# Optimization experiments

Measured on AMD Instinct MI355X. Metric: run time of the kernel, lower is better.

The kernel has to match this reference:

```python
import jax, jax.numpy as jnp
import numpy as np

DIM = 192
TDIM = 192
HEADS = 6
WS = (2, 7, 7)
SS = (1, 3, 3)
MLP_HID = 4 * DIM
RANK = DIM // 8
EPS = 1e-6


def _rel_pos_index(ws):
    wd, wh, ww = ws
    coords = np.stack(np.meshgrid(np.arange(wd), np.arange(wh), np.arange(ww), indexing='ij'))
    cf = coords.reshape(3, -1)
    rel = (cf[:, :, None] - cf[:, None, :]).transpose(1, 2, 0).astype(np.int64)
    rel[..., 0] += wd - 1
    rel[..., 1] += wh - 1
    rel[..., 2] += ww - 1
    rel[..., 0] *= (2 * wh - 1) * (2 * ww - 1)
    rel[..., 1] *= (2 * ww - 1)
    return rel.sum(-1)  # (N, N)


def _window_partition(x, ws):
    B, D, H, W, C = x.shape
    x = x.reshape(B, D // ws[0], ws[0], H // ws[1], ws[1], W // ws[2], ws[2], C)
    return x.transpose(0, 1, 3, 5, 2, 4, 6, 7).reshape(-1, ws[0] * ws[1] * ws[2], C)


def _window_reverse(w, ws, B, D, H, W):
    x = w.reshape(B, D // ws[0], H // ws[1], W // ws[2], ws[0], ws[1], ws[2], -1)
    return x.transpose(0, 1, 4, 2, 5, 3, 6, 7).reshape(B, D, H, W, -1)


def _ln(x):
    m = x.mean(-1, keepdims=True)
    v = ((x - m) ** 2).mean(-1, keepdims=True)
    return (x - m) * jax.lax.rsqrt(v + EPS)


def _compute_mask_np(Dp, Hp, Wp, ws, ss):
    img = np.zeros((1, Dp, Hp, Wp, 1), dtype=np.float32)
    cnt = 0
    for d in (slice(0, -ws[0]), slice(-ws[0], -ss[0]), slice(-ss[0], None)):
        for h in (slice(0, -ws[1]), slice(-ws[1], -ss[1]), slice(-ss[1], None)):
            for w in (slice(0, -ws[2]), slice(-ws[2], -ss[2]), slice(-ss[2], None)):
                img[:, d, h, w, :] = cnt
                cnt += 1
    x = img.reshape(1, Dp // ws[0], ws[0], Hp // ws[1], ws[1], Wp // ws[2], ws[2], 1)
    mw = x.transpose(0, 1, 3, 5, 2, 4, 6, 7).reshape(-1, ws[0] * ws[1] * ws[2])
    am = mw[:, None, :] - mw[:, :, None]
    return np.where(am != 0, np.float32(-100.0), np.float32(0.0))


def setup_inputs() -> dict:
    key = jax.random.key(0)
    ks = jax.random.split(key, 16)
    B, D, H, W, C = 1, 16, 64, 128, DIM
    Dp = D + (-D) % WS[0]
    Hp = H + (-H) % WS[1]
    Wp = W + (-W) % WS[2]
    s = 0.02
    bias_tab = (2 * WS[0] - 1) * (2 * WS[1] - 1) * (2 * WS[2] - 1)
    return {
        'x': jax.random.normal(ks[0], (B, D, H, W, C), jnp.float32),
        'mask_matrix': jnp.asarray(_compute_mask_np(Dp, Hp, Wp, WS, SS)),
        't': jax.random.normal(ks[1], (B, TDIM), jnp.float32),
        'w_qkv': jax.random.normal(ks[2], (C, 3 * C), jnp.float32) * s,
        'b_qkv': jnp.zeros((3 * C,), jnp.float32),
        'rel_bias': jax.random.normal(ks[3], (bias_tab, HEADS), jnp.float32) * s,
        'w_proj': jax.random.normal(ks[4], (C, C), jnp.float32) * s,
        'b_proj': jnp.zeros((C,), jnp.float32),
        'w1': jax.random.normal(ks[5], (C, MLP_HID), jnp.float32) * s,
        'b1': jnp.zeros((MLP_HID,), jnp.float32),
        'w2': jax.random.normal(ks[6], (MLP_HID, C), jnp.float32) * s,
        'b2': jnp.zeros((C,), jnp.float32),
        'wa1': jax.random.normal(ks[7], (TDIM, RANK), jnp.float32) * s,
        'wa2': jax.random.normal(ks[8], (RANK, 6 * C), jnp.float32) * s,
        'ba2': jax.random.normal(ks[9], (6 * C,), jnp.float32) * s,
    }


def reference(x, mask_matrix, t, w_qkv, b_qkv, rel_bias, w_proj, b_proj, w1, b1, w2, b2, wa1, wa2, ba2):
    B, D, H, W, C = x.shape
    hd = C // HEADS
    # AdaLN modulation params
    mod = (jax.nn.silu(t) @ wa1) @ wa2 + ba2  # (B, 6C)
    sh_msa, sc_msa, g_msa, sh_mlp, sc_mlp, g_mlp = jnp.split(mod, 6, axis=1)

    def modulate(y, sh, sc):
        return y * (1 + sc[:, None, None, None, :]) + sh[:, None, None, None, :]

    shortcut = x
    y = modulate(_ln(x), sh_msa, sc_msa)
    # pad to window multiples
    pad_d, pad_h, pad_w = (-D) % WS[0], (-H) % WS[1], (-W) % WS[2]
    y = jnp.pad(y, ((0, 0), (0, pad_d), (0, pad_h), (0, pad_w), (0, 0)))
    Dp, Hp, Wp = D + pad_d, H + pad_h, W + pad_w
    # cyclic shift
    y = jnp.roll(y, (-SS[0], -SS[1], -SS[2]), axis=(1, 2, 3))
    xw = _window_partition(y, WS)  # (B*nW, N, C)
    N = xw.shape[1]
    qkv = (xw @ w_qkv + b_qkv).reshape(-1, N, 3, HEADS, hd)
    q, k, v = qkv[:, :, 0], qkv[:, :, 1], qkv[:, :, 2]
    scale = hd ** -0.5
    attn = jnp.einsum('bnhd,bmhd->bhnm', q * scale, k)  # (B*nW, H, N, N)
    rpi = _rel_pos_index(WS)
    bias = rel_bias[rpi.reshape(-1)].reshape(N, N, HEADS).transpose(2, 0, 1)
    attn = attn + bias[None]
    nW = mask_matrix.shape[0]
    attn = attn.reshape(B, nW, HEADS, N, N) + mask_matrix[None, :, None]
    attn = jax.nn.softmax(attn, axis=-1).reshape(-1, HEADS, N, N)
    out = jnp.einsum('bhnm,bmhd->bnhd', attn, v).reshape(-1, N, C)
    out = out @ w_proj + b_proj
    y = _window_reverse(out, WS, B, Dp, Hp, Wp)
    y = jnp.roll(y, (SS[0], SS[1], SS[2]), axis=(1, 2, 3))
    y = y[:, :D, :H, :W, :]
    x1 = shortcut + g_msa[:, None, None, None, :] * y
    y2 = modulate(_ln(x1), sh_mlp, sc_mlp)
    h = jax.nn.gelu(y2 @ w1 + b1, approximate=False) @ w2 + b2
    return x1 + g_mlp[:, None, None, None, :] * h
```

## Files before the change

kernel.cpp:

```cpp
#include <hip/hip_runtime.h>
#include <hip/hip_bf16.h>

typedef __bf16 bf16x8 __attribute__((ext_vector_type(8)));
typedef float  f32x4  __attribute__((ext_vector_type(4)));
typedef unsigned int u32x4 __attribute__((ext_vector_type(4)));
typedef __attribute__((address_space(3))) unsigned int lds_u32;
typedef const __attribute__((address_space(1))) unsigned int glb_u32;

__device__ inline unsigned short f2bf(float f) {
    union { __hip_bfloat16 h; unsigned short u; } cv;
    cv.h = __float2bfloat16(f);
    return cv.u;
}
__device__ inline float bf2f(unsigned short u) {
    union { unsigned int i; float f; } c; c.i = ((unsigned int)u) << 16; return c.f;
}

__device__ inline bf16x8 load8(const unsigned short* p) {
    uint2 lo = *(const uint2*)(p);
    uint2 hi = *(const uint2*)(p + 16);
    u32x4 v; v[0] = lo.x; v[1] = lo.y; v[2] = hi.x; v[3] = hi.y;
    return __builtin_bit_cast(bf16x8, v);
}

__device__ inline bf16x8 load8s(const unsigned short* rowbase, int lg, int r3) {
    int b0 = ((((lg >> 1)    ) ^ r3) << 4) + ((lg & 1) << 3);
    int b1 = ((((lg >> 1) + 2) ^ r3) << 4) + ((lg & 1) << 3);
    uint2 lo = *(const uint2*)((const char*)rowbase + b0);
    uint2 hi = *(const uint2*)((const char*)rowbase + b1);
    u32x4 v; v[0] = lo.x; v[1] = lo.y; v[2] = hi.x; v[3] = hi.y;
    return __builtin_bit_cast(bf16x8, v);
}

__device__ inline f32x4 mfma16(bf16x8 a, bf16x8 b, f32x4 c) {
    return __builtin_amdgcn_mfma_f32_16x16x32_bf16(a, b, c, 0, 0, 0);
}

__device__ inline bool winmapT(int gg, int& T) {
    int win = gg / 98, n = gg % 98;
    int wdi = win / 190, rem = win % 190, whi = rem / 19, wwi = rem % 19;
    int td = n / 49, th = (n / 7) % 7, tw = n % 7;
    int sd = (wdi * 2 + td + 1) & 15;
    int sh = whi * 7 + th + 3; if (sh >= 70) sh -= 70;
    int sw = wwi * 7 + tw + 3; if (sw >= 133) sw -= 133;
    if (sh < 64 && sw < 128) { T = (sd * 64 + sh) * 128 + sw; return true; }
    return false;
}

__device__ inline int xcd_swz(int orig, int nwg) {
    int q = nwg >> 3, r = nwg & 7;
    int xcd = orig & 7, idx = orig >> 3;
    return (xcd < r ? xcd * (q + 1) : r * (q + 1) + (xcd - r) * q) + idx;
}

__global__ __launch_bounds__(256) void mod_k(const float* __restrict__ t,
    const float* __restrict__ wa1, const float* __restrict__ wa2,
    const float* __restrict__ ba2, float* __restrict__ mod)
{
    __shared__ float st[192];
    __shared__ float a[24];
    int tid = threadIdx.x;
    if (tid < 192) { float x = t[tid]; st[tid] = x / (1.f + __expf(-x)); }
    __syncthreads();
    if (tid < 24) {
        float s = 0.f;
        for (int c = 0; c < 192; ++c) s += st[c] * wa1[c * 24 + tid];
        a[tid] = s;
    }
    __syncthreads();
    for (int j = tid; j < 1152; j += 256) {
        float s = ba2[j];
        for (int r = 0; r < 24; ++r) s += a[r] * wa2[r * 1152 + j];
        mod[j] = s;
    }
}

__global__ __launch_bounds__(256) void prep_k(
    const float* __restrict__ wqkv, const float* __restrict__ bqkv,
    const float* __restrict__ wproj,
    const float* __restrict__ w1, const float* __restrict__ w2,
    const float* __restrict__ relb,
    unsigned short* __restrict__ wqkvH, float* __restrict__ bqkvH,
    unsigned short* __restrict__ wprojT,
    unsigned short* __restrict__ w1T, unsigned short* __restrict__ w2T,
    unsigned short* __restrict__ btabF)
{
    int i = blockIdx.x * 256 + threadIdx.x;
    if (i < 110592) {
        int h = i / 18432, r = i % 18432, c96 = r / 192, k = r % 192;
        int which = c96 >> 5, c = c96 & 31;
        wqkvH[i] = f2bf(wqkv[k * 576 + which * 192 + h * 32 + c]);
        return;
    }
    i -= 110592;
    if (i < 36864)  { int n = i / 192, k = i % 192; wprojT[i] = f2bf(wproj[k * 192 + n]); return; }
    i -= 36864;
    if (i < 147456) { int n = i / 192, k = i % 192; w1T[i] = f2bf(w1[k * 768 + n]); return; }
    i -= 147456;
    if (i < 147456) { int n = i / 768, k = i % 768; w2T[i] = f2bf(w2[k * 192 + n]); return; }
    i -= 147456;
    if (i < 688128) {
        int mt = i / 86016, r1 = i % 86016;
        int h  = r1 / 14336, r2 = r1 % 14336;
        int fq = r2 / 2048,  r3 = r2 % 2048;
        int l16 = r3 / 128,  r4 = r3 % 128;
        int lg  = r4 / 32,   r5 = r4 % 32;
        int fkey = r5 / 4,   e  = r5 % 4;
        int q = fq * 16 + l16, key = fkey * 16 + lg * 4 + e;
        float val;
        if (fkey == 7 || q >= 98 || key >= 98) {
            val = -1e30f;
        } else {
            int tdn = q / 49, thn = (q / 7) % 7, twn = q % 7;
            int tdm = key / 49, thm = (key / 7) % 7, twm = key % 7;
            int idx = (tdn - tdm + 1) * 169 + (thn - thm + 6) * 13 + (twn - twm + 6);
            float b = relb[idx * 6 + h];
            int bd = mt & 1, bh = (mt >> 1) & 1, bw = (mt >> 2) & 1;
            int idn = (bd ? (tdn == 0 ? 1 : 2) : 0) * 9 + (bh ? (thn < 4 ? 1 : 2) : 0) * 3 + (bw ? (twn < 4 ? 1 : 2) : 0);
            int idm = (bd ? (tdm == 0 ? 1 : 2) : 0) * 9 + (bh ? (thm < 4 ? 1 : 2) : 0) * 3 + (bw ? (twm < 4 ? 1 : 2) : 0);
            val = b + ((idn != idm) ? -100.f : 0.f);
        }
        btabF[i] = f2bf(val);
        return;
    }
    i -= 688128;
    if (i < 576) {
        int h = i / 96, c96 = i % 96;
        int which = c96 >> 5, c = c96 & 31;
        bqkvH[i] = bqkv[which * 192 + h * 32 + c];
    }
}

__global__ __launch_bounds__(256) void lnwin_k(const float* __restrict__ x,
    const float* __restrict__ mod, unsigned short* __restrict__ ywin)
{
    int tok = blockIdx.x * 4 + (threadIdx.x >> 6);
    int lane = threadIdx.x & 63;
    int T;
    size_t ob = (size_t)tok * 192;
    if (winmapT(tok, T)) {
        const float* p = x + (size_t)T * 192;
        float x0 = p[lane], xa = p[64 + lane], xb = p[128 + lane];
        float s = x0 + xa + xb, q = x0 * x0 + xa * xa + xb * xb;
        for (int m = 32; m; m >>= 1) { s += __shfl_xor(s, m); q += __shfl_xor(q, m); }
        float mean = s * (1.f / 192.f);
        float var  = q * (1.f / 192.f) - mean * mean;
        float rstd = rsqrtf(var + 1e-6f);
        ywin[ob + lane]       = f2bf((x0 - mean) * rstd * (1.f + mod[192 + lane])       + mod[lane]);
        ywin[ob + 64 + lane]  = f2bf((xa - mean) * rstd * (1.f + mod[192 + 64 + lane])  + mod[64 + lane]);
        ywin[ob + 128 + lane] = f2bf((xb - mean) * rstd * (1.f + mod[192 + 128 + lane]) + mod[128 + lane]);
    } else {
        ywin[ob + lane] = 0; ywin[ob + 64 + lane] = 0; ywin[ob + 128 + lane] = 0;
    }
}

__global__ __launch_bounds__(256) void ln2_k(const float* __restrict__ x1,
    const float* __restrict__ mod, unsigned short* __restrict__ y2)
{
    int tok = blockIdx.x * 4 + (threadIdx.x >> 6);
    int lane = threadIdx.x & 63;
    const float* p = x1 + (size_t)tok * 192;
    float x0 = p[lane], xa = p[64 + lane], xb = p[128 + lane];
    float s = x0 + xa + xb, q = x0 * x0 + xa * xa + xb * xb;
    for (int m = 32; m; m >>= 1) { s += __shfl_xor(s, m); q += __shfl_xor(q, m); }
    float mean = s * (1.f / 192.f);
    float var  = q * (1.f / 192.f) - mean * mean;
    float rstd = rsqrtf(var + 1e-6f);
    size_t ob = (size_t)tok * 192;
    y2[ob + lane]       = f2bf((x0 - mean) * rstd * (1.f + mod[768 + lane])       + mod[576 + lane]);
    y2[ob + 64 + lane]  = f2bf((xa - mean) * rstd * (1.f + mod[768 + 64 + lane])  + mod[576 + 64 + lane]);
    y2[ob + 128 + lane] = f2bf((xb - mean) * rstd * (1.f + mod[768 + 128 + lane]) + mod[576 + 128 + lane]);
}

template<int FN, int EPI>
__global__ __launch_bounds__(256) void gemm_k(
    const unsigned short* __restrict__ A, const unsigned short* __restrict__ BT,
    const float* __restrict__ bias, unsigned short* __restrict__ outB, float* outF,
    const float* __restrict__ auxF, const float* __restrict__ mod,
    int M, int N, int K, int nx)
{
    constexpr int BN = FN * 32;
    __shared__ unsigned short As[2][128 * 32];
    __shared__ unsigned short Bs[2][BN * 32];
    const int t = threadIdx.x;
    const int wg = xcd_swz(blockIdx.x, gridDim.x);
    const int n0 = (wg % nx) * BN, m0 = (wg / nx) * 128;
    const int wid = t >> 6, lane = t & 63;
    const int lg = lane >> 4, l16 = lane & 15;
    const int wm = (wid >> 1) * 64, wn = (wid & 1) * (FN * 16);
    f32x4 acc[4][FN] = {};

    int arow[2], acs[2];
    #pragma unroll
    for (int j = 0; j < 2; ++j) {
        int p = t + j * 256;
        arow[j] = p >> 2;
        acs[j] = (p & 3) ^ (arow[j] & 3);
    }
    const unsigned short* asrc[2];
    const unsigned short* bsrc[BN / 64];
    #pragma unroll
    for (int j = 0; j < 2; ++j) {
        int gr = m0 + arow[j];
        asrc[j] = A + (size_t)(gr < M ? gr : 0) * K + acs[j] * 8;
    }
    #pragma unroll
    for (int j = 0; j < BN / 64; ++j) {
        int gn = n0 + arow[j];
        bsrc[j] = BT + (size_t)(gn < N ? gn : 0) * K + acs[j] * 8;
    }

    const int NS = K >> 5;

    #pragma unroll
    for (int j = 0; j < 2; ++j)
        __builtin_amdgcn_global_load_lds((glb_u32*)(asrc[j]),
            (lds_u32*)((char*)&As[0][0] + wid * 1024 + j * 4096), 16, 0, 0);
    #pragma unroll
    for (int j = 0; j < BN / 64; ++j)
        __builtin_amdgcn_global_load_lds((glb_u32*)(bsrc[j]),
            (lds_u32*)((char*)&Bs[0][0] + wid * 1024 + j * 4096), 16, 0, 0);
    __syncthreads();

    for (int s = 0; s < NS; ++s) {
        const int cur = s & 1;
        if (s + 1 < NS) {
            const int kk = (s + 1) << 5;
            #pragma unroll
            for (int j = 0; j < 2; ++j)
                __builtin_amdgcn_global_load_lds((glb_u32*)(asrc[j] + kk),
                    (lds_u32*)((char*)&As[cur ^ 1][0] + wid * 1024 + j * 4096), 16, 0, 0);
            #pragma unroll
            for (int j = 0; j < BN / 64; ++j)
                __builtin_amdgcn_global_load_lds((glb_u32*)(bsrc[j] + kk),
                    (lds_u32*)((char*)&Bs[cur ^ 1][0] + wid * 1024 + j * 4096), 16, 0, 0);
        }
        bf16x8 af[4], bv[FN];
        #pragma unroll
        for (int i = 0; i < 4; ++i) {
            int r = wm + i * 16 + l16;
            af[i] = load8s(&As[cur][r * 32], lg, r & 3);
        }
        #pragma unroll
        for (int j = 0; j < FN; ++j) {
            int r = wn + j * 16 + l16;
            bv[j] = load8s(&Bs[cur][r * 32], lg, r & 3);
        }
        #pragma unroll
        for (int i = 0; i < 4; ++i)
        #pragma unroll
        for (int j = 0; j < FN; ++j)
            acc[i][j] = mfma16(af[i], bv[j], acc[i][j]);
        __syncthreads();
    }

    #pragma unroll
    for (int i = 0; i < 4; ++i)
    #pragma unroll
    for (int j = 0; j < FN; ++j) {
        int gcol = n0 + wn + j * 16 + l16;
        if (gcol >= N) continue;
        float b = bias[gcol];
        #pragma unroll
        for (int e = 0; e < 4; ++e) {
            int grow = m0 + wm + i * 16 + lg * 4 + e;
            if (grow >= M) continue;
            float v = acc[i][j][e] + b;
            if (EPI == 1) {
                float gl = 0.5f * v * (1.f + erff(v * 0.70710678118654752f));
                outB[(size_t)grow * N + gcol] = f2bf(gl);
            } else if (EPI == 2) {
                int T;
                if (winmapT(grow, T)) {
                    size_t idx = (size_t)T * 192 + gcol;
                    outF[idx] = auxF[idx] + mod[384 + gcol] * v;
                }
            } else {
                size_t idx = (size_t)grow * 192 + gcol;
                outF[idx] = outF[idx] + mod[960 + gcol] * v;
            }
        }
    }
}

__global__ __launch_bounds__(256) void qkvattn_k(
    const unsigned short* __restrict__ ywin, const unsigned short* __restrict__ wqkvH,
    const float* __restrict__ bqkvH, const unsigned short* __restrict__ btabF,
    unsigned short* __restrict__ out)
{
    __shared__ unsigned short As[128 * 196];
    __shared__ unsigned short Bs[96 * 196];
    __shared__ unsigned short Qs[112 * 46];
    __shared__ unsigned short Ks[112 * 46];
    __shared__ unsigned short VT[32 * 142];

    const int win = xcd_swz(blockIdx.x, 1520);
    const int t = threadIdx.x;
    const int wid = t >> 6, lane = t & 63;
    const int lg = lane >> 4, l16 = lane & 15;
    const int wr = wid >> 1, wc = wid & 1;
    const size_t rb = (size_t)win * 98;

    const int wdi = win / 190, remw = win % 190, whi = remw / 19, wwi = remw % 19;
    const int mt = (wdi == 7 ? 1 : 0) | (whi == 9 ? 2 : 0) | (wwi == 18 ? 4 : 0);
    const float SCALE = 0.17677669529663687f;

    for (int p = t; p < 128 * 24; p += 256) {
        int row = p / 24, ch = p % 24;
        uint4 w = make_uint4(0u, 0u, 0u, 0u);
        if (row < 98) w = *(const uint4*)(ywin + (rb + row) * 192 + ch * 8);
        *(uint2*)(&As[row * 196 + ch * 8])     = make_uint2(w.x, w.y);
        *(uint2*)(&As[row * 196 + ch * 8 + 4]) = make_uint2(w.z, w.w);
    }

    for (int h = 0; h < 6; ++h) {
        const unsigned short* Wh = wqkvH + (size_t)h * 96 * 192;
        for (int p = t; p < 96 * 24; p += 256) {
            int row = p / 24, ch = p % 24;
            uint4 w = *(const uint4*)(Wh + row * 192 + ch * 8);
            *(uint2*)(&Bs[row * 196 + ch * 8])     = make_uint2(w.x, w.y);
            *(uint2*)(&Bs[row * 196 + ch * 8 + 4]) = make_uint2(w.z, w.w);
        }
        __syncthreads();

        __builtin_amdgcn_s_setprio(1);
        f32x4 acc[4][3] = {};
        #pragma unroll
        for (int kb = 0; kb < 6; ++kb) {
            bf16x8 af[4], bv[3];
            #pragma unroll
            for (int i2 = 0; i2 < 4; ++i2)
                af[i2] = load8(&As[(wr * 64 + i2 * 16 + l16) * 196 + kb * 32 + 4 * lg]);
            #pragma unroll
            for (int j = 0; j < 3; ++j)
                bv[j] = load8(&Bs[(wc * 48 + j * 16 + l16) * 196 + kb * 32 + 4 * lg]);
            #pragma unroll
            for (int i2 = 0; i2 < 4; ++i2)
            #pragma unroll
            for (int j = 0; j < 3; ++j)
                acc[i2][j] = mfma16(af[i2], bv[j], acc[i2][j]);
        }
        __builtin_amdgcn_s_setprio(0);

        #pragma unroll
        for (int j = 0; j < 3; ++j) {
            int c96 = wc * 48 + j * 16 + l16;
            float bb = bqkvH[h * 96 + c96];
            int which = c96 >> 5, c = c96 & 31;
            #pragma unroll
            for (int i2 = 0; i2 < 4; ++i2)
            #pragma unroll
            for (int e = 0; e < 4; ++e) {
                int row = wr * 64 + i2 * 16 + lg * 4 + e;
                unsigned short val = f2bf(acc[i2][j][e] + bb);
                if (which == 0)      { if (row < 112) Qs[row * 46 + c] = val; }
                else if (which == 1) { if (row < 112) Ks[row * 46 + c] = val; }
                else                 { VT[c * 142 + row] = val; }
            }
        }
        __syncthreads();

        const unsigned short* btW = btabF + (size_t)(mt * 6 + h) * 14336;
        #pragma unroll
        for (int fi = 0; fi < 2; ++fi) {
            const int fq = wid + fi * 4;
            if (fq >= 7) break;

            const uint4* bp = (const uint4*)(btW + fq * 2048 + l16 * 128 + lg * 32);
            uint4 b0 = bp[0], b1 = bp[1], b2 = bp[2], b3 = bp[3];
            const unsigned bt32[16] = {b0.x, b0.y, b0.z, b0.w, b1.x, b1.y, b1.z, b1.w,
                                       b2.x, b2.y, b2.z, b2.w, b3.x, b3.y, b3.z, b3.w};

            bf16x8 qa = load8(Qs + (fq * 16 + l16) * 46 + 4 * lg);
            f32x4 sc[7];
            #pragma unroll
            for (int fk = 0; fk < 7; ++fk) {
                bf16x8 kb = load8(Ks + (fk * 16 + l16) * 46 + 4 * lg);
                f32x4 z = {};
                sc[fk] = mfma16(kb, qa, z);
            }

            float mx = -1e30f;
            #pragma unroll
            for (int fk = 0; fk < 7; ++fk)
            #pragma unroll
            for (int e = 0; e < 4; ++e) {
                unsigned short bu = (unsigned short)(bt32[fk * 2 + (e >> 1)] >> ((e & 1) * 16));
                float s = fmaf(sc[fk][e], SCALE, bf2f(bu));
                sc[fk][e] = s;
                mx = fmaxf(mx, s);
            }
            mx = fmaxf(mx, __shfl_xor(mx, 16));
            mx = fmaxf(mx, __shfl_xor(mx, 32));
            float sum = 0.f;
            #pragma unroll
            for (int fk = 0; fk < 7; ++fk)
            #pragma unroll
            for (int e = 0; e < 4; ++e) {
                float p = __expf(sc[fk][e] - mx);
                sc[fk][e] = p;
                sum += p;
            }
            sum += __shfl_xor(sum, 16);
            sum += __shfl_xor(sum, 32);
            float rinv = 1.f / sum;

            bf16x8 sa[4];
            #pragma unroll
            for (int ks = 0; ks < 4; ++ks) {
                u32x4 w;
                w[0] = (unsigned)f2bf(sc[2 * ks][0]) | ((unsigned)f2bf(sc[2 * ks][1]) << 16);
                w[1] = (unsigned)f2bf(sc[2 * ks][2]) | ((unsigned)f2bf(sc[2 * ks][3]) << 16);
                if (ks < 3) {
                    w[2] = (unsigned)f2bf(sc[2 * ks + 1][0]) | ((unsigned)f2bf(sc[2 * ks + 1][1]) << 16);
                    w[3] = (unsigned)f2bf(sc[2 * ks + 1][2]) | ((unsigned)f2bf(sc[2 * ks + 1][3]) << 16);
                } else {
                    w[2] = 0u; w[3] = 0u;
                }
                sa[ks] = __builtin_bit_cast(bf16x8, w);
            }
            float rv[4];
            #pragma unroll
            for (int e = 0; e < 4; ++e) rv[e] = __shfl(rinv, lg * 4 + e);

            #pragma unroll
            for (int fn = 0; fn < 2; ++fn) {
                f32x4 o = {};
                #pragma unroll
                for (int ks = 0; ks < 4; ++ks) {
                    bf16x8 vb = load8(VT + (fn * 16 + l16) * 142 + ks * 32 + 4 * lg);
                    o = mfma16(sa[ks], vb, o);
                }
                #pragma unroll
                for (int e = 0; e < 4; ++e) {
                    int r = fq * 16 + lg * 4 + e;
                    if (r < 98) {
                        out[(rb + r) * 192 + h * 32 + fn * 16 + l16] = f2bf(o[e] * rv[e]);
                    }
                }
            }
        }
    }
}

extern "C" void kernel_launch(void* const* d_in, const int* in_sizes, int n_in,
                              void* d_out, int out_size, void* d_ws, size_t ws_size,
                              hipStream_t stream)
{
    const float* x      = (const float*)d_in[0];
    const float* tvec   = (const float*)d_in[2];
    const float* w_qkv  = (const float*)d_in[3];
    const float* b_qkv  = (const float*)d_in[4];
    const float* relb   = (const float*)d_in[5];
    const float* w_proj = (const float*)d_in[6];
    const float* b_proj = (const float*)d_in[7];
    const float* w1     = (const float*)d_in[8];
    const float* b1     = (const float*)d_in[9];
    const float* w2     = (const float*)d_in[10];
    const float* b2     = (const float*)d_in[11];
    const float* wa1    = (const float*)d_in[12];
    const float* wa2    = (const float*)d_in[13];
    const float* ba2    = (const float*)d_in[14];

    char* ws = (char*)d_ws;
    float*          mod    = (float*)ws;
    float*          bqkvH  = (float*)(ws + 4608);
    unsigned short* wqkvH  = (unsigned short*)(ws + 2101760);
    unsigned short* wprojT = (unsigned short*)(ws + 2322944);
    unsigned short* w1T    = (unsigned short*)(ws + 2396672);
    unsigned short* w2T    = (unsigned short*)(ws + 2691584);
    unsigned short* btabF  = (unsigned short*)(ws + 2986496);
    unsigned short* h      = (unsigned short*)(ws + 4834304);
    unsigned short* attn_c = (unsigned short*)(ws + 176436224);
    unsigned short* ywin   = (unsigned short*)(ws + 233636864);
    unsigned short* y2b    = (unsigned short*)(ws + 290837504);
    float*          dout   = (float*)d_out;

    mod_k<<<1, 256, 0, stream>>>(tvec, wa1, wa2, ba2, mod);
    prep_k<<<4418, 256, 0, stream>>>(w_qkv, b_qkv, w_proj, w1, w2, relb,
                                     wqkvH, bqkvH, wprojT, w1T, w2T, btabF);
    lnwin_k<<<37240, 256, 0, stream>>>(x, mod, ywin);

    qkvattn_k<<<1520, 256, 0, stream>>>(ywin, wqkvH, bqkvH, btabF, attn_c);
    gemm_k<2, 2><<<3 * 1164, 256, 0, stream>>>(
        attn_c, wprojT, b_proj, nullptr, dout, x, mod, 148960, 192, 192, 3);

    ln2_k<<<32768, 256, 0, stream>>>(dout, mod, y2b);

    gemm_k<4, 1><<<6 * 1024, 256, 0, stream>>>(
        y2b, w1T, b1, h, nullptr, nullptr, mod, 131072, 768, 192, 6);
    gemm_k<2, 3><<<3 * 1024, 256, 0, stream>>>(
        h, w2T, b2, nullptr, dout, nullptr, mod, 131072, 192, 768, 3);
}
```

Baseline: 1.005 ms.

## Keep per-head QKV weights in registers and shrink LDS for two blocks per CU

The per-head QKV weight tile is no longer staged through shared memory. Each thread loads its fragments straight from global memory into registers, and the next head's fragments are prefetched after the attention phase. The A tile shrinks from 128 to 112 rows and the dead 16-row MFMA tile is skipped, which cuts LDS use so that launch_bounds(256,2) can fit two blocks per CU. The cost is higher register pressure from the 18 bf16x8 weight fragments, which may cause spills under the tighter register budget, plus uncoalesced global loads.

```diff
diff --git a/kernel.cpp b/kernel.cpp
--- a/kernel.cpp
+++ b/kernel.cpp
@@ -283,13 +283,12 @@
     }
 }
 
-__global__ __launch_bounds__(256) void qkvattn_k(
+__global__ __launch_bounds__(256, 2) void qkvattn_k(
     const unsigned short* __restrict__ ywin, const unsigned short* __restrict__ wqkvH,
     const float* __restrict__ bqkvH, const unsigned short* __restrict__ btabF,
     unsigned short* __restrict__ out)
 {
-    __shared__ unsigned short As[128 * 196];
-    __shared__ unsigned short Bs[96 * 196];
+    __shared__ unsigned short As[112 * 196];
     __shared__ unsigned short Qs[112 * 46];
     __shared__ unsigned short Ks[112 * 46];
     __shared__ unsigned short VT[32 * 142];
@@ -305,7 +304,11 @@
     const int mt = (wdi == 7 ? 1 : 0) | (whi == 9 ? 2 : 0) | (wwi == 18 ? 4 : 0);
     const float SCALE = 0.17677669529663687f;
 
-    for (int p = t; p < 128 * 24; p += 256) {
+    for (int i = t; i < 32 * 16; i += 256) {
+        int c = i >> 4, m = 112 + (i & 15);
+        VT[c * 142 + m] = 0;
+    }
+    for (int p = t; p < 112 * 24; p += 256) {
         int row = p / 24, ch = p % 24;
         uint4 w = make_uint4(0u, 0u, 0u, 0u);
         if (row < 98) w = *(const uint4*)(ywin + (rb + row) * 192 + ch * 8);
@@ -313,32 +316,33 @@
         *(uint2*)(&As[row * 196 + ch * 8 + 4]) = make_uint2(w.z, w.w);
     }
 
+    bf16x8 breg[3][6];
+    {
+        const unsigned short* Wh = wqkvH;
+        #pragma unroll
+        for (int j = 0; j < 3; ++j)
+        #pragma unroll
+        for (int kb = 0; kb < 6; ++kb)
+            breg[j][kb] = load8(Wh + (wc * 48 + j * 16 + l16) * 192 + kb * 32 + 4 * lg);
+    }
+    __syncthreads();
+
     for (int h = 0; h < 6; ++h) {
-        const unsigned short* Wh = wqkvH + (size_t)h * 96 * 192;
-        for (int p = t; p < 96 * 24; p += 256) {
-            int row = p / 24, ch = p % 24;
-            uint4 w = *(const uint4*)(Wh + row * 192 + ch * 8);
-            *(uint2*)(&Bs[row * 196 + ch * 8])     = make_uint2(w.x, w.y);
-            *(uint2*)(&Bs[row * 196 + ch * 8 + 4]) = make_uint2(w.z, w.w);
-        }
-        __syncthreads();
-
         __builtin_amdgcn_s_setprio(1);
         f32x4 acc[4][3] = {};
         #pragma unroll
         for (int kb = 0; kb < 6; ++kb) {
-            bf16x8 af[4], bv[3];
+            bf16x8 af[4];
             #pragma unroll
             for (int i2 = 0; i2 < 4; ++i2)
-                af[i2] = load8(&As[(wr * 64 + i2 * 16 + l16) * 196 + kb * 32 + 4 * lg]);
+                if (wr == 0 || i2 < 3)
+                    af[i2] = load8(&As[(wr * 64 + i2 * 16 + l16) * 196 + kb * 32 + 4 * lg]);
+            #pragma unroll
+            for (int i2 = 0; i2 < 4; ++i2)
             #pragma unroll
             for (int j = 0; j < 3; ++j)
-                bv[j] = load8(&Bs[(wc * 48 + j * 16 + l16) * 196 + kb * 32 + 4 * lg]);
-            #pragma unroll
-            for (int i2 = 0; i2 < 4; ++i2)
-            #pragma unroll
-            for (int j = 0; j < 3; ++j)
-                acc[i2][j] = mfma16(af[i2], bv[j], acc[i2][j]);
+                if (wr == 0 || i2 < 3)
+                    acc[i2][j] = mfma16(af[i2], breg[j][kb], acc[i2][j]);
         }
         __builtin_amdgcn_s_setprio(0);
 
@@ -348,14 +352,16 @@
             float bb = bqkvH[h * 96 + c96];
             int which = c96 >> 5, c = c96 & 31;
             #pragma unroll
-            for (int i2 = 0; i2 < 4; ++i2)
-            #pragma unroll
-            for (int e = 0; e < 4; ++e) {
-                int row = wr * 64 + i2 * 16 + lg * 4 + e;
-                unsigned short val = f2bf(acc[i2][j][e] + bb);
-                if (which == 0)      { if (row < 112) Qs[row * 46 + c] = val; }
-                else if (which == 1) { if (row < 112) Ks[row * 46 + c] = val; }
-                else                 { VT[c * 142 + row] = val; }
+            for (int i2 = 0; i2 < 4; ++i2) {
+                if (wr == 1 && i2 == 3) continue;
+                #pragma unroll
+                for (int e = 0; e < 4; ++e) {
+                    int row = wr * 64 + i2 * 16 + lg * 4 + e;
+                    unsigned short val = f2bf(acc[i2][j][e] + bb);
+                    if (which == 0)      Qs[row * 46 + c] = val;
+                    else if (which == 1) Ks[row * 46 + c] = val;
+                    else                 VT[c * 142 + row] = val;
+                }
             }
         }
         __syncthreads();
@@ -440,6 +446,16 @@
                 }
             }
         }
+
+        if (h < 5) {
+            const unsigned short* Wh = wqkvH + (size_t)(h + 1) * 96 * 192;
+            #pragma unroll
+            for (int j = 0; j < 3; ++j)
+            #pragma unroll
+            for (int kb = 0; kb < 6; ++kb)
+                breg[j][kb] = load8(Wh + (wc * 48 + j * 16 + l16) * 192 + kb * 32 + 4 * lg);
+        }
+        __syncthreads();
     }
 }
 
```

Result: faster. 905.5 us (-9.9%).
